# Kernel tuning notes

Measured on AMD Instinct MI355X. Metric: run time of the kernel, lower is better.

The kernel has to match this reference:

```python
import jax, jax.numpy as jnp
import numpy as np

IN_DIM = 512
HID = IN_DIM // 2
N_SCENES = 64
SEG_LEN = 4096
N = N_SCENES * SEG_LEN
EPS = 1e-5


def setup_inputs() -> dict:
    key = jax.random.key(0)
    ks = jax.random.split(key, 6)
    feats = jax.random.normal(ks[0], (N, IN_DIM), dtype=jnp.float32)
    offsets = (jnp.arange(N_SCENES + 1, dtype=jnp.int32) * SEG_LEN)
    ln_g = jnp.ones((IN_DIM,), jnp.float32) + 0.02 * jax.random.normal(ks[1], (IN_DIM,), jnp.float32)
    ln_b = 0.02 * jax.random.normal(ks[2], (IN_DIM,), jnp.float32)
    w1 = jax.random.normal(ks[3], (HID, IN_DIM), jnp.float32) / np.sqrt(IN_DIM)
    b1 = jnp.zeros((HID,), jnp.float32)
    w2 = jax.random.normal(ks[4], (1, HID), jnp.float32) / np.sqrt(HID)
    b2 = jnp.zeros((1,), jnp.float32)
    return {"feats": feats, "ln_g": ln_g, "ln_b": ln_b, "w1": w1, "b1": b1, "w2": w2, "b2": b2, "offsets": offsets}


def reference(feats, ln_g, ln_b, w1, b1, w2, b2, offsets):
    n = feats.shape[0]
    # segment id per point from prefix-sum offsets
    seg = jnp.searchsorted(offsets, jnp.arange(n, dtype=offsets.dtype), side="right") - 1
    # score MLP: LayerNorm -> Linear -> GELU(exact) -> Linear -> scalar
    mu = jnp.mean(feats, axis=-1, keepdims=True)
    var = jnp.mean(jnp.square(feats - mu), axis=-1, keepdims=True)
    x = (feats - mu) * jax.lax.rsqrt(var + EPS) * ln_g + ln_b
    h = jax.nn.gelu(x @ w1.T + b1, approximate=False)  # [N, HID]
    s = (h @ w2.T + b2)[:, 0]  # [N]
    # segment softmax (stable)
    smax = jax.ops.segment_max(s, seg, num_segments=N_SCENES)
    e = jnp.exp(s - smax[seg])
    denom = jax.ops.segment_sum(e, seg, num_segments=N_SCENES)
    w = e / denom[seg]
    # weighted sum per segment -> [N_SCENES, IN_DIM]
    pooled = jax.ops.segment_sum(feats * w[:, None], seg, num_segments=N_SCENES)
    return pooled
```

## Files before the change

kernel.cpp:

```cpp
#include <hip/hip_runtime.h>

#define IN_DIM 512
#define HID_DIM 256
#define XS_STRIDE 520

typedef __bf16 bf16x8 __attribute__((ext_vector_type(8)));
typedef unsigned short ushort8 __attribute__((ext_vector_type(8)));
typedef float floatx4 __attribute__((ext_vector_type(4)));

__device__ __forceinline__ unsigned short f2bf_rne(float x) {
    unsigned int u = __float_as_uint(x);
    u += 0x7FFFu + ((u >> 16) & 1u);
    return (unsigned short)(u >> 16);
}

__device__ __forceinline__ unsigned int pack_bf2(float lo, float hi) {
    const unsigned int u0 = __float_as_uint(lo) + 0x8000u;
    const unsigned int u1 = __float_as_uint(hi) + 0x8000u;
    return __builtin_amdgcn_perm(u1, u0, 0x07060302u);
}

__global__ void prep_w1_kernel(const float* __restrict__ w1, const float* __restrict__ ln_g,
                               const float* __restrict__ ln_b, const float* __restrict__ b1,
                               unsigned short* __restrict__ w1g, float* __restrict__ gw,
                               float* __restrict__ c1) {
    const int wid = threadIdx.x >> 6;
    const int lane = threadIdx.x & 63;
    const int h = blockIdx.x * 4 + wid;
    const int c8 = lane * 8;
    const float4 wv0 = *(const float4*)(w1 + (size_t)h * IN_DIM + c8);
    const float4 wv1 = *(const float4*)(w1 + (size_t)h * IN_DIM + c8 + 4);
    const float4 g0 = *(const float4*)(ln_g + c8);
    const float4 g1 = *(const float4*)(ln_g + c8 + 4);
    const float4 bb0 = *(const float4*)(ln_b + c8);
    const float4 bb1 = *(const float4*)(ln_b + c8 + 4);
    float wg[8] = {wv0.x * g0.x, wv0.y * g0.y, wv0.z * g0.z, wv0.w * g0.w,
                   wv1.x * g1.x, wv1.y * g1.y, wv1.z * g1.z, wv1.w * g1.w};
    float sg = wg[0] + wg[1] + wg[2] + wg[3] + wg[4] + wg[5] + wg[6] + wg[7];
    float sb = wv0.x * bb0.x + wv0.y * bb0.y + wv0.z * bb0.z + wv0.w * bb0.w +
               wv1.x * bb1.x + wv1.y * bb1.y + wv1.z * bb1.z + wv1.w * bb1.w;
    ushort8 outv;
#pragma unroll
    for (int j = 0; j < 8; j++) outv[j] = f2bf_rne(wg[j]);
    *(ushort8*)(w1g + (size_t)h * IN_DIM + c8) = outv;
    for (int m = 32; m; m >>= 1) {
        sg += __shfl_xor(sg, m);
        sb += __shfl_xor(sb, m);
    }
    if (lane == 0) {
        gw[h] = sg;
        c1[h] = sb + b1[h];
    }
}

__global__ __launch_bounds__(256, 2) void score_kernel(
    const float* __restrict__ feats, const unsigned short* __restrict__ w1g,
    const float* __restrict__ gw, const float* __restrict__ c1,
    const float* __restrict__ w2, const float* __restrict__ b2,
    float* __restrict__ s_out, int N) {
    __shared__ unsigned short xs[64][XS_STRIDE];
    __shared__ float spart[4][64];
    __shared__ float2 stats_s[64];

    const int tid = threadIdx.x;
    const int wid = tid >> 6;
    const int lane = tid & 63;
    const int quad = lane >> 4;
    const int l16 = lane & 15;
    const int row0 = blockIdx.x * 64;
    const int c8 = lane * 8;

#pragma unroll 4
    for (int i = 0; i < 16; i += 2) {
        const int ra = (wid << 4) + i;
        size_t rowa = (size_t)(row0 + ra);
        size_t rowb = rowa + 1;
        if (rowa >= (size_t)N) rowa = (size_t)N - 1;
        if (rowb >= (size_t)N) rowb = (size_t)N - 1;
        const float4 a0 = *(const float4*)(feats + rowa * IN_DIM + c8);
        const float4 a1 = *(const float4*)(feats + rowa * IN_DIM + c8 + 4);
        const float4 d0 = *(const float4*)(feats + rowb * IN_DIM + c8);
        const float4 d1 = *(const float4*)(feats + rowb * IN_DIM + c8 + 4);
        uint4 pa, pb;
        pa.x = pack_bf2(a0.x, a0.y);
        pa.y = pack_bf2(a0.z, a0.w);
        pa.z = pack_bf2(a1.x, a1.y);
        pa.w = pack_bf2(a1.z, a1.w);
        pb.x = pack_bf2(d0.x, d0.y);
        pb.y = pack_bf2(d0.z, d0.w);
        pb.z = pack_bf2(d1.x, d1.y);
        pb.w = pack_bf2(d1.z, d1.w);
        *(uint4*)&xs[ra][c8] = pa;
        *(uint4*)&xs[ra + 1][c8] = pb;
    }
    __syncthreads();

    floatx4 acc[4][4];
#pragma unroll
    for (int rt = 0; rt < 4; rt++)
#pragma unroll
        for (int ht = 0; ht < 4; ht++) acc[rt][ht] = (floatx4)(0.0f);

    float sumf = 0.0f, sumq = 0.0f;
    const int hbase = wid * 64;
    for (int kk = 0; kk < IN_DIM; kk += 32) {
        const int kc = kk + quad * 8;
        ushort8 au[4];
        bf16x8 bf[4];
#pragma unroll
        for (int rt = 0; rt < 4; rt++) {
            au[rt] = *(const ushort8*)&xs[rt * 16 + l16][kc];
            if (rt == wid) {
                const unsigned int* p = (const unsigned int*)&au[rt];
#pragma unroll
                for (int d = 0; d < 4; d++) {
                    const float lo = __uint_as_float(p[d] << 16);
                    const float hi = __uint_as_float(p[d] & 0xffff0000u);
                    sumf += lo + hi;
                    sumq += lo * lo + hi * hi;
                }
            }
        }
#pragma unroll
        for (int ht = 0; ht < 4; ht++) {
            const int hid = hbase + ht * 16 + l16;
            bf[ht] = __builtin_bit_cast(bf16x8, *(const ushort8*)(w1g + hid * IN_DIM + kc));
        }
#pragma unroll
        for (int rt = 0; rt < 4; rt++)
#pragma unroll
            for (int ht = 0; ht < 4; ht++)
                acc[rt][ht] = __builtin_amdgcn_mfma_f32_16x16x32_bf16(
                    __builtin_bit_cast(bf16x8, au[rt]), bf[ht], acc[rt][ht], 0, 0, 0);
    }

    sumf += __shfl_xor(sumf, 16);
    sumf += __shfl_xor(sumf, 32);
    sumq += __shfl_xor(sumq, 16);
    sumq += __shfl_xor(sumq, 32);
    if (lane < 16) {
        const float mu = sumf * (1.0f / IN_DIM);
        const float var = fmaxf(sumq * (1.0f / IN_DIM) - mu * mu, 0.0f);
        stats_s[(wid << 4) + lane] = make_float2(mu, rsqrtf(var + 1e-5f));
    }
    __syncthreads();

    float gwv[4], c1v[4], w2v[4];
#pragma unroll
    for (int ht = 0; ht < 4; ht++) {
        const int hid = hbase + ht * 16 + l16;
        gwv[ht] = gw[hid];
        c1v[ht] = c1[hid];
        w2v[ht] = w2[hid];
    }
    float2 st[4][4];
#pragma unroll
    for (int rt = 0; rt < 4; rt++)
#pragma unroll
        for (int reg = 0; reg < 4; reg++) st[rt][reg] = stats_s[rt * 16 + quad * 4 + reg];

    float p[4][4];
#pragma unroll
    for (int rt = 0; rt < 4; rt++) {
#pragma unroll
        for (int reg = 0; reg < 4; reg++) {
            const float mu = st[rt][reg].x, rs = st[rt][reg].y;
            float t = 0.0f;
#pragma unroll
            for (int ht = 0; ht < 4; ht++) {
                const float hv = rs * (acc[rt][ht][reg] - mu * gwv[ht]) + c1v[ht];
                t += 0.5f * hv * (1.0f + erff(hv * 0.70710678118654752f)) * w2v[ht];
            }
            p[rt][reg] = t;
        }
    }
#pragma unroll
    for (int m = 1; m < 16; m <<= 1)
#pragma unroll
        for (int rt = 0; rt < 4; rt++)
#pragma unroll
            for (int reg = 0; reg < 4; reg++) p[rt][reg] += __shfl_xor(p[rt][reg], m);
    if (l16 == 0) {
#pragma unroll
        for (int rt = 0; rt < 4; rt++)
#pragma unroll
            for (int reg = 0; reg < 4; reg++)
                spart[wid][rt * 16 + quad * 4 + reg] = p[rt][reg];
    }
    __syncthreads();
    if (tid < 64) {
        const int row = row0 + tid;
        if (row < N)
            s_out[row] = spart[0][tid] + spart[1][tid] + spart[2][tid] + spart[3][tid] + b2[0];
    }
}

__global__ void segstat_kernel(const float* __restrict__ s, const int* __restrict__ offsets,
                               float* __restrict__ smax, float* __restrict__ denom, int nseg) {
    const int seg = blockIdx.x;
    const int st = offsets[seg];
    const int en = offsets[seg + 1];
    const int tid = threadIdx.x;
    __shared__ float red[8];
    float m = -3.4e38f;
    for (int i = st + tid; i < en; i += 256) m = fmaxf(m, s[i]);
    for (int mm = 32; mm; mm >>= 1) m = fmaxf(m, __shfl_xor(m, mm));
    if ((tid & 63) == 0) red[tid >> 6] = m;
    __syncthreads();
    const float M = fmaxf(fmaxf(red[0], red[1]), fmaxf(red[2], red[3]));
    float sum = 0.0f;
    for (int i = st + tid; i < en; i += 256) sum += expf(s[i] - M);
    for (int mm = 32; mm; mm >>= 1) sum += __shfl_xor(sum, mm);
    if ((tid & 63) == 0) red[4 + (tid >> 6)] = sum;
    __syncthreads();
    if (tid == 0) {
        smax[seg] = M;
        denom[seg] = red[4] + red[5] + red[6] + red[7];
    }
}

#define CHUNK 256
__global__ __launch_bounds__(256) void pool_kernel(
    const float* __restrict__ feats, const float* __restrict__ s,
    const float* __restrict__ smax, const float* __restrict__ denom,
    const int* __restrict__ offsets, int nseg, float* __restrict__ out, int N) {
    __shared__ float wbuf[CHUNK];
    __shared__ int sbuf[CHUNK];
    const int tid = threadIdx.x;
    const int r0 = blockIdx.x * CHUNK;
    const int nrows = min(CHUNK, N - r0);

    {
        const int row = r0 + tid;
        float wv = 0.0f;
        int sg = 0;
        if (row < N) {
            int lo = 0, hi = nseg;
            while (hi - lo > 1) {
                const int mid = (lo + hi) >> 1;
                if (offsets[mid] <= row) lo = mid; else hi = mid;
            }
            sg = lo;
            wv = expf(s[row] - smax[sg]) / denom[sg];
        }
        wbuf[tid] = wv;
        sbuf[tid] = sg;
    }
    __syncthreads();

    const int seg0 = sbuf[0];
    const int segl = sbuf[nrows - 1];
    const int d = 2 * tid;
    if (seg0 == segl) {
        float ax = 0.0f, ay = 0.0f;
        const float* fp = feats + (size_t)r0 * IN_DIM + d;
#pragma unroll 8
        for (int r = 0; r < nrows; r++) {
            const float2 f = *(const float2*)(fp + (size_t)r * IN_DIM);
            const float wv = wbuf[r];
            ax += wv * f.x;
            ay += wv * f.y;
        }
        atomicAdd(&out[seg0 * IN_DIM + d], ax);
        atomicAdd(&out[seg0 * IN_DIM + d + 1], ay);
    } else {
        for (int r = 0; r < nrows; r++) {
            const float2 f = *(const float2*)(feats + (size_t)(r0 + r) * IN_DIM + d);
            const float wv = wbuf[r];
            const int sg = sbuf[r];
            if (wv != 0.0f) {
                atomicAdd(&out[sg * IN_DIM + d], wv * f.x);
                atomicAdd(&out[sg * IN_DIM + d + 1], wv * f.y);
            }
        }
    }
}

extern "C" void kernel_launch(void* const* d_in, const int* in_sizes, int n_in,
                              void* d_out, int out_size, void* d_ws, size_t ws_size,
                              hipStream_t stream) {
    const float* feats = (const float*)d_in[0];
    const float* ln_g = (const float*)d_in[1];
    const float* ln_b = (const float*)d_in[2];
    const float* w1 = (const float*)d_in[3];
    const float* b1 = (const float*)d_in[4];
    const float* w2 = (const float*)d_in[5];
    const float* b2 = (const float*)d_in[6];
    const int* offsets = (const int*)d_in[7];
    const int N = in_sizes[0] / IN_DIM;
    const int nseg = in_sizes[7] - 1;
    float* out = (float*)d_out;

    char* ws = (char*)d_ws;
    unsigned short* w1g = (unsigned short*)ws;
    float* gw = (float*)(ws + (size_t)HID_DIM * IN_DIM * 2);
    float* c1 = gw + HID_DIM;
    float* s_arr = c1 + HID_DIM;
    float* smax = s_arr + N;
    float* denom = smax + nseg;

    hipMemsetAsync(d_out, 0, (size_t)out_size * sizeof(float), stream);
    prep_w1_kernel<<<HID_DIM / 4, 256, 0, stream>>>(w1, ln_g, ln_b, b1, w1g, gw, c1);
    score_kernel<<<(N + 63) / 64, 256, 0, stream>>>(feats, w1g, gw, c1, w2, b2, s_arr, N);
    segstat_kernel<<<nseg, 256, 0, stream>>>(s_arr, offsets, smax, denom, nseg);
    pool_kernel<<<(N + CHUNK - 1) / CHUNK, 256, 0, stream>>>(feats, s_arr, smax, denom, offsets, nseg, out, N);
}
```

Baseline: 941.0 us.

## Make score kernel persistent with register-resident W1 and 32x32 MFMA tiles

The score kernel becomes a persistent 512-thread kernel. Each wave keeps its 32-hidden slice of the bf16 W1 in registers for all tiles and uses 32x32x16 MFMAs over 32-row tiles. LayerNorm statistics are now computed in fp32 during the global load, and exact erf GELU is replaced with a polynomial approximation. The pool kernel moves to float4 loads, with the block split into two row halves, to cut per-row load instructions. The risks are high register pressure from the 32 bf16x8 weight fragments, extra syncs per tile, a small change in accuracy from the GELU approximation, and twice as many atomics in the pool kernel.

Measured after the change: 901.9 us. 1.04x faster.

```diff
diff --git a/kernel.cpp b/kernel.cpp
--- a/kernel.cpp
+++ b/kernel.cpp
@@ -2,22 +2,34 @@
 
 #define IN_DIM 512
 #define HID_DIM 256
-#define XS_STRIDE 520
+#define ROWS 32
+#define XSS 520
 
 typedef __bf16 bf16x8 __attribute__((ext_vector_type(8)));
 typedef unsigned short ushort8 __attribute__((ext_vector_type(8)));
-typedef float floatx4 __attribute__((ext_vector_type(4)));
+typedef float floatx16 __attribute__((ext_vector_type(16)));
 
 __device__ __forceinline__ unsigned short f2bf_rne(float x) {
     unsigned int u = __float_as_uint(x);
     u += 0x7FFFu + ((u >> 16) & 1u);
     return (unsigned short)(u >> 16);
 }
-
 __device__ __forceinline__ unsigned int pack_bf2(float lo, float hi) {
     const unsigned int u0 = __float_as_uint(lo) + 0x8000u;
     const unsigned int u1 = __float_as_uint(hi) + 0x8000u;
     return __builtin_amdgcn_perm(u1, u0, 0x07060302u);
+}
+__device__ __forceinline__ float gelu(float x) {
+    const float ax = fabsf(x) * 0.70710678118654752f;
+    const float t = __builtin_amdgcn_rcpf(1.0f + 0.3275911f * ax);
+    const float y = t * (0.254829592f +
+                    t * (-0.284496736f +
+                    t * (1.421413741f +
+                    t * (-1.453152027f + t * 1.061405429f))));
+    const float e = __expf(-ax * ax);
+    float er = 1.0f - y * e;
+    er = __builtin_copysignf(er, x);
+    return 0.5f * x * (1.0f + er);
 }
 
 __global__ void prep_w1_kernel(const float* __restrict__ w1, const float* __restrict__ ln_g,
@@ -53,145 +65,114 @@
     }
 }
 
-__global__ __launch_bounds__(256, 2) void score_kernel(
+__global__ __launch_bounds__(512, 2) void score_kernel(
     const float* __restrict__ feats, const unsigned short* __restrict__ w1g,
     const float* __restrict__ gw, const float* __restrict__ c1,
     const float* __restrict__ w2, const float* __restrict__ b2,
-    float* __restrict__ s_out, int N) {
-    __shared__ unsigned short xs[64][XS_STRIDE];
-    __shared__ float spart[4][64];
-    __shared__ float2 stats_s[64];
+    float* __restrict__ s_out, int N, int ntiles) {
+    __shared__ unsigned short xs[ROWS][XSS];
+    __shared__ float2 stats_s[ROWS];
+    __shared__ float spart[8][ROWS];
 
     const int tid = threadIdx.x;
     const int wid = tid >> 6;
     const int lane = tid & 63;
-    const int quad = lane >> 4;
-    const int l16 = lane & 15;
-    const int row0 = blockIdx.x * 64;
-    const int c8 = lane * 8;
-
-#pragma unroll 4
-    for (int i = 0; i < 16; i += 2) {
-        const int ra = (wid << 4) + i;
-        size_t rowa = (size_t)(row0 + ra);
-        size_t rowb = rowa + 1;
-        if (rowa >= (size_t)N) rowa = (size_t)N - 1;
-        if (rowb >= (size_t)N) rowb = (size_t)N - 1;
-        const float4 a0 = *(const float4*)(feats + rowa * IN_DIM + c8);
-        const float4 a1 = *(const float4*)(feats + rowa * IN_DIM + c8 + 4);
-        const float4 d0 = *(const float4*)(feats + rowb * IN_DIM + c8);
-        const float4 d1 = *(const float4*)(feats + rowb * IN_DIM + c8 + 4);
-        uint4 pa, pb;
-        pa.x = pack_bf2(a0.x, a0.y);
-        pa.y = pack_bf2(a0.z, a0.w);
-        pa.z = pack_bf2(a1.x, a1.y);
-        pa.w = pack_bf2(a1.z, a1.w);
-        pb.x = pack_bf2(d0.x, d0.y);
-        pb.y = pack_bf2(d0.z, d0.w);
-        pb.z = pack_bf2(d1.x, d1.y);
-        pb.w = pack_bf2(d1.z, d1.w);
-        *(uint4*)&xs[ra][c8] = pa;
-        *(uint4*)&xs[ra + 1][c8] = pb;
-    }
-    __syncthreads();
-
-    floatx4 acc[4][4];
-#pragma unroll
-    for (int rt = 0; rt < 4; rt++)
-#pragma unroll
-        for (int ht = 0; ht < 4; ht++) acc[rt][ht] = (floatx4)(0.0f);
-
-    float sumf = 0.0f, sumq = 0.0f;
-    const int hbase = wid * 64;
-    for (int kk = 0; kk < IN_DIM; kk += 32) {
-        const int kc = kk + quad * 8;
-        ushort8 au[4];
-        bf16x8 bf[4];
-#pragma unroll
-        for (int rt = 0; rt < 4; rt++) {
-            au[rt] = *(const ushort8*)&xs[rt * 16 + l16][kc];
-            if (rt == wid) {
-                const unsigned int* p = (const unsigned int*)&au[rt];
-#pragma unroll
-                for (int d = 0; d < 4; d++) {
-                    const float lo = __uint_as_float(p[d] << 16);
-                    const float hi = __uint_as_float(p[d] & 0xffff0000u);
-                    sumf += lo + hi;
-                    sumq += lo * lo + hi * hi;
-                }
-            }
-        }
-#pragma unroll
-        for (int ht = 0; ht < 4; ht++) {
-            const int hid = hbase + ht * 16 + l16;
-            bf[ht] = __builtin_bit_cast(bf16x8, *(const ushort8*)(w1g + hid * IN_DIM + kc));
-        }
-#pragma unroll
-        for (int rt = 0; rt < 4; rt++)
-#pragma unroll
-            for (int ht = 0; ht < 4; ht++)
-                acc[rt][ht] = __builtin_amdgcn_mfma_f32_16x16x32_bf16(
-                    __builtin_bit_cast(bf16x8, au[rt]), bf[ht], acc[rt][ht], 0, 0, 0);
-    }
-
-    sumf += __shfl_xor(sumf, 16);
-    sumf += __shfl_xor(sumf, 32);
-    sumq += __shfl_xor(sumq, 16);
-    sumq += __shfl_xor(sumq, 32);
-    if (lane < 16) {
-        const float mu = sumf * (1.0f / IN_DIM);
-        const float var = fmaxf(sumq * (1.0f / IN_DIM) - mu * mu, 0.0f);
-        stats_s[(wid << 4) + lane] = make_float2(mu, rsqrtf(var + 1e-5f));
-    }
-    __syncthreads();
-
-    float gwv[4], c1v[4], w2v[4];
-#pragma unroll
-    for (int ht = 0; ht < 4; ht++) {
-        const int hid = hbase + ht * 16 + l16;
-        gwv[ht] = gw[hid];
-        c1v[ht] = c1[hid];
-        w2v[ht] = w2[hid];
-    }
-    float2 st[4][4];
-#pragma unroll
-    for (int rt = 0; rt < 4; rt++)
-#pragma unroll
-        for (int reg = 0; reg < 4; reg++) st[rt][reg] = stats_s[rt * 16 + quad * 4 + reg];
-
-    float p[4][4];
-#pragma unroll
-    for (int rt = 0; rt < 4; rt++) {
-#pragma unroll
-        for (int reg = 0; reg < 4; reg++) {
-            const float mu = st[rt][reg].x, rs = st[rt][reg].y;
-            float t = 0.0f;
-#pragma unroll
-            for (int ht = 0; ht < 4; ht++) {
-                const float hv = rs * (acc[rt][ht][reg] - mu * gwv[ht]) + c1v[ht];
-                t += 0.5f * hv * (1.0f + erff(hv * 0.70710678118654752f)) * w2v[ht];
-            }
-            p[rt][reg] = t;
-        }
-    }
-#pragma unroll
-    for (int m = 1; m < 16; m <<= 1)
-#pragma unroll
-        for (int rt = 0; rt < 4; rt++)
-#pragma unroll
-            for (int reg = 0; reg < 4; reg++) p[rt][reg] += __shfl_xor(p[rt][reg], m);
-    if (l16 == 0) {
-#pragma unroll
-        for (int rt = 0; rt < 4; rt++)
-#pragma unroll
-            for (int reg = 0; reg < 4; reg++)
-                spart[wid][rt * 16 + quad * 4 + reg] = p[rt][reg];
-    }
-    __syncthreads();
-    if (tid < 64) {
-        const int row = row0 + tid;
-        if (row < N)
-            s_out[row] = spart[0][tid] + spart[1][tid] + spart[2][tid] + spart[3][tid] + b2[0];
+    const int l31 = lane & 31;
+    const int hi = lane >> 5;
+    const int hid = wid * 32 + l31;
+
+    const float gwv = gw[hid];
+    const float c1v = c1[hid];
+    const float w2v = w2[hid];
+    const float b2v = b2[0];
+
+    bf16x8 barr[32];
+    {
+        const unsigned short* bp = w1g + (size_t)hid * IN_DIM + hi * 8;
+#pragma unroll
+        for (int ki = 0; ki < 32; ki++)
+            barr[ki] = __builtin_bit_cast(bf16x8, *(const ushort8*)(bp + ki * 16));
+    }
+
+    const int srow = tid >> 4;
+    const int schunk = tid & 15;
+
+    for (int t = blockIdx.x; t < ntiles; t += gridDim.x) {
+        const int row0 = t * ROWS;
+
+        {
+            size_t rg = (size_t)(row0 + srow);
+            if (rg >= (size_t)N) rg = (size_t)N - 1;
+            const float* fp = feats + rg * IN_DIM + schunk * 4;
+            float4 f[8];
+#pragma unroll
+            for (int j = 0; j < 8; j++) f[j] = *(const float4*)(fp + j * 64);
+            float sf = 0.0f, qf = 0.0f;
+#pragma unroll
+            for (int j = 0; j < 8; j++) {
+                sf += f[j].x + f[j].y + f[j].z + f[j].w;
+                qf = fmaf(f[j].x, f[j].x, qf);
+                qf = fmaf(f[j].y, f[j].y, qf);
+                qf = fmaf(f[j].z, f[j].z, qf);
+                qf = fmaf(f[j].w, f[j].w, qf);
+            }
+#pragma unroll
+            for (int j = 0; j < 8; j++) {
+                uint2 p;
+                p.x = pack_bf2(f[j].x, f[j].y);
+                p.y = pack_bf2(f[j].z, f[j].w);
+                *(uint2*)&xs[srow][j * 64 + schunk * 4] = p;
+            }
+#pragma unroll
+            for (int m = 1; m < 16; m <<= 1) {
+                sf += __shfl_xor(sf, m);
+                qf += __shfl_xor(qf, m);
+            }
+            if (schunk == 0) {
+                const float mu = sf * (1.0f / IN_DIM);
+                const float var = fmaxf(qf * (1.0f / IN_DIM) - mu * mu, 0.0f);
+                stats_s[srow] = make_float2(mu, rsqrtf(var + 1e-5f));
+            }
+        }
+        __syncthreads();
+
+        floatx16 acc = (floatx16)(0.0f);
+        {
+            const unsigned short* ap = &xs[l31][hi * 8];
+#pragma unroll
+            for (int ki = 0; ki < 32; ki++) {
+                const bf16x8 af = __builtin_bit_cast(bf16x8, *(const ushort8*)(ap + ki * 16));
+                acc = __builtin_amdgcn_mfma_f32_32x32x16_bf16(af, barr[ki], acc, 0, 0, 0);
+            }
+        }
+
+        float tv[16];
+#pragma unroll
+        for (int r = 0; r < 16; r++) {
+            const int row = (r & 3) + 8 * (r >> 2) + 4 * hi;
+            const float2 st = stats_s[row];
+            const float hv = st.y * (acc[r] - st.x * gwv) + c1v;
+            tv[r] = gelu(hv) * w2v;
+        }
+#pragma unroll
+        for (int m = 1; m < 32; m <<= 1)
+#pragma unroll
+            for (int r = 0; r < 16; r++) tv[r] += __shfl_xor(tv[r], m);
+        if (l31 == 0) {
+#pragma unroll
+            for (int r = 0; r < 16; r++)
+                spart[wid][(r & 3) + 8 * (r >> 2) + 4 * hi] = tv[r];
+        }
+        __syncthreads();
+        if (tid < ROWS) {
+            const int row = row0 + tid;
+            if (row < N) {
+                float sv = b2v;
+#pragma unroll
+                for (int w = 0; w < 8; w++) sv += spart[w][tid];
+                s_out[row] = sv;
+            }
+        }
     }
 }
 
@@ -235,10 +216,10 @@
         float wv = 0.0f;
         int sg = 0;
         if (row < N) {
-            int lo = 0, hi = nseg;
-            while (hi - lo > 1) {
-                const int mid = (lo + hi) >> 1;
-                if (offsets[mid] <= row) lo = mid; else hi = mid;
+            int lo = 0, hiq = nseg;
+            while (hiq - lo > 1) {
+                const int mid = (lo + hiq) >> 1;
+                if (offsets[mid] <= row) lo = mid; else hiq = mid;
             }
             sg = lo;
             wv = expf(s[row] - smax[sg]) / denom[sg];
@@ -248,30 +229,39 @@
     }
     __syncthreads();
 
-    const int seg0 = sbuf[0];
-    const int segl = sbuf[nrows - 1];
-    const int d = 2 * tid;
-    if (seg0 == segl) {
-        float ax = 0.0f, ay = 0.0f;
-        const float* fp = feats + (size_t)r0 * IN_DIM + d;
-#pragma unroll 8
-        for (int r = 0; r < nrows; r++) {
-            const float2 f = *(const float2*)(fp + (size_t)r * IN_DIM);
+    const int c4 = (tid & 127) * 4;
+    const int half = tid >> 7;
+    const int rs = half * (CHUNK / 2);
+    const int re = min(rs + CHUNK / 2, nrows);
+    if (re <= rs) return;
+
+    if (sbuf[0] == sbuf[nrows - 1]) {
+        const int seg = sbuf[0];
+        float ax = 0.0f, ay = 0.0f, az = 0.0f, aw = 0.0f;
+        const float* fp = feats + (size_t)r0 * IN_DIM + c4;
+#pragma unroll 4
+        for (int r = rs; r < re; r++) {
+            const float4 f = *(const float4*)(fp + (size_t)r * IN_DIM);
             const float wv = wbuf[r];
-            ax += wv * f.x;
-            ay += wv * f.y;
-        }
-        atomicAdd(&out[seg0 * IN_DIM + d], ax);
-        atomicAdd(&out[seg0 * IN_DIM + d + 1], ay);
+            ax = fmaf(wv, f.x, ax);
+            ay = fmaf(wv, f.y, ay);
+            az = fmaf(wv, f.z, az);
+            aw = fmaf(wv, f.w, aw);
+        }
+        float* op = out + (size_t)seg * IN_DIM + c4;
+        atomicAdd(op + 0, ax);
+        atomicAdd(op + 1, ay);
+        atomicAdd(op + 2, az);
+        atomicAdd(op + 3, aw);
     } else {
-        for (int r = 0; r < nrows; r++) {
-            const float2 f = *(const float2*)(feats + (size_t)(r0 + r) * IN_DIM + d);
+        for (int r = rs; r < re; r++) {
+            const float4 f = *(const float4*)(feats + (size_t)(r0 + r) * IN_DIM + c4);
             const float wv = wbuf[r];
-            const int sg = sbuf[r];
-            if (wv != 0.0f) {
-                atomicAdd(&out[sg * IN_DIM + d], wv * f.x);
-                atomicAdd(&out[sg * IN_DIM + d + 1], wv * f.y);
-            }
+            float* op = out + (size_t)sbuf[r] * IN_DIM + c4;
+            atomicAdd(op + 0, wv * f.x);
+            atomicAdd(op + 1, wv * f.y);
+            atomicAdd(op + 2, wv * f.z);
+            atomicAdd(op + 3, wv * f.w);
         }
     }
 }
@@ -299,9 +289,12 @@
     float* smax = s_arr + N;
     float* denom = smax + nseg;
 
+    const int ntiles = (N + ROWS - 1) / ROWS;
+    int sgrid = ntiles < 2048 ? ntiles : 2048;
+
     hipMemsetAsync(d_out, 0, (size_t)out_size * sizeof(float), stream);
     prep_w1_kernel<<<HID_DIM / 4, 256, 0, stream>>>(w1, ln_g, ln_b, b1, w1g, gw, c1);
-    score_kernel<<<(N + 63) / 64, 256, 0, stream>>>(feats, w1g, gw, c1, w2, b2, s_arr, N);
+    score_kernel<<<sgrid, 512, 0, stream>>>(feats, w1g, gw, c1, w2, b2, s_arr, N, ntiles);
     segstat_kernel<<<nseg, 256, 0, stream>>>(s_arr, offsets, smax, denom, nseg);
     pool_kernel<<<(N + CHUNK - 1) / CHUNK, 256, 0, stream>>>(feats, s_arr, smax, denom, offsets, nseg, out, N);
 }
```
